# Kernel optimization log

Measured on AMD Instinct MI355X. Metric: run time of the kernel, lower is better.

The kernel has to match this reference:

```python
import jax, jax.numpy as jnp
import numpy as np

B, N, C = 8, 1024, 768
H = 12
HD = C // H
RANK = 8
SCALE = HD ** -0.5


def setup_inputs() -> dict:
    key = jax.random.key(0)
    ks = jax.random.split(key, 12)
    s = C ** -0.5
    inp = {
        'x': jax.random.normal(ks[0], (B, N, C), jnp.float32),
        'w_qkv': jax.random.normal(ks[1], (3 * C, C), jnp.float32) * s,
        'b_qkv': jax.random.normal(ks[2], (3 * C,), jnp.float32) * 0.02,
        'w_proj': jax.random.normal(ks[3], (C, C), jnp.float32) * s,
        'b_proj': jax.random.normal(ks[4], (C,), jnp.float32) * 0.02,
        # LoRA A matrices (kaiming-uniform-ish); B matrices are zero at init,
        # but use small nonzero values so the adapter path is exercised.
        'q_a': jax.random.normal(ks[5], (RANK, C), jnp.float32) * s,
        'q_b': jax.random.normal(ks[6], (C, RANK), jnp.float32) * 0.01,
        'k_a': jax.random.normal(ks[7], (RANK, C), jnp.float32) * s,
        'k_b': jax.random.normal(ks[8], (C, RANK), jnp.float32) * 0.01,
        'v_a': jax.random.normal(ks[9], (RANK, C), jnp.float32) * s,
        'v_b': jax.random.normal(ks[10], (C, RANK), jnp.float32) * 0.01,
        'o_a': jax.random.normal(ks[11], (RANK, C), jnp.float32) * s,
        'o_b': jax.random.normal(jax.random.fold_in(key, 99), (C, RANK), jnp.float32) * 0.01,
    }
    return inp


def _lora(x, wa, wb):
    # x:[B,N,C], wa:[r,C], wb:[C,r] -> [B,N,C]
    return jnp.einsum('bnr,cr->bnc', jnp.einsum('bnc,rc->bnr', x, wa), wb)


def reference(x, w_qkv, b_qkv, w_proj, b_proj, q_a, q_b, k_a, k_b, v_a, v_b, o_a, o_b):
    # QKV projection + fused LoRA slice-adds
    qkv = jnp.einsum('bnc,dc->bnd', x, w_qkv) + b_qkv  # [B,N,3C]
    q = qkv[:, :, :C] + _lora(x, q_a, q_b)
    k = qkv[:, :, C:2 * C] + _lora(x, k_a, k_b)
    v = qkv[:, :, 2 * C:] + _lora(x, v_a, v_b)
    # [B,H,N,HD]
    q = q.reshape(B, N, H, HD).transpose(0, 2, 1, 3)
    k = k.reshape(B, N, H, HD).transpose(0, 2, 1, 3)
    v = v.reshape(B, N, H, HD).transpose(0, 2, 1, 3)
    attn = jnp.einsum('bhqd,bhkd->bhqk', q, k) * SCALE
    attn = jax.nn.softmax(attn, axis=-1)  # dropout is identity in eval
    o = jnp.einsum('bhqk,bhkd->bhqd', attn, v)
    o = o.transpose(0, 2, 1, 3).reshape(B, N, C)
    out = jnp.einsum('bnc,dc->bnd', o, w_proj) + b_proj + _lora(o, o_a, o_b)
    return out
```

## Files before the change

### kernel.cpp

```cpp
#include <hip/hip_runtime.h>

typedef __attribute__((ext_vector_type(8))) short short8;
typedef __attribute__((ext_vector_type(4))) float f32x4;
typedef __attribute__((ext_vector_type(4))) unsigned short u16x4;
typedef __attribute__((ext_vector_type(2))) unsigned int u32x2;

#define MFMA16(a,b,c) __builtin_amdgcn_mfma_f32_16x16x32_bf16((a),(b),(c),0,0,0)

#define QSCALE 0.1803368801f

__device__ __forceinline__ unsigned short f2bf(float f) {
  unsigned int x = __float_as_uint(f);
  x += 0x7fffu + ((x >> 16) & 1u);
  return (unsigned short)(x >> 16);
}
__device__ __forceinline__ unsigned int pack2bf(float a, float b) {
  unsigned int ua = __float_as_uint(a) + 0x8000u;
  unsigned int ub = __float_as_uint(b) + 0x8000u;
  return __builtin_amdgcn_perm(ub, ua, 0x07060302);
}
__device__ __forceinline__ void gload16(const unsigned short* g, unsigned short* l) {
  __builtin_amdgcn_global_load_lds(
      (const __attribute__((address_space(1))) unsigned int*)g,
      (__attribute__((address_space(3))) unsigned int*)l, 16, 0, 0);
}

__global__ __launch_bounds__(256) void prep(
    const float* __restrict__ x,
    const float* __restrict__ w_qkv,
    const float* __restrict__ w_proj,
    const float* __restrict__ q_a, const float* __restrict__ q_b,
    const float* __restrict__ k_a, const float* __restrict__ k_b,
    const float* __restrict__ v_a, const float* __restrict__ v_b,
    const float* __restrict__ o_a, const float* __restrict__ o_b,
    unsigned short* __restrict__ xb,
    unsigned short* __restrict__ wqkv_eff,
    unsigned short* __restrict__ wproj_eff)
{
  int bid = blockIdx.x;
  if (bid < 6144) {
    int i4 = (bid * 256 + threadIdx.x) * 4;
    f32x4 v = *(const f32x4*)&x[i4];
    u16x4 o;
    o.x = f2bf(v.x); o.y = f2bf(v.y); o.z = f2bf(v.z); o.w = f2bf(v.w);
    *(u16x4*)&xb[i4] = o;
    return;
  }
  const int QKV = 2304 * 768;
  int idx = (bid - 6144) * 256 + threadIdx.x;
  if (idx < QKV) {
    int n = idx / 768, c = idx - n * 768;
    int sec = n / 768;
    int nr = n - sec * 768;
    const float* a; const float* b;
    if (sec == 0)      { a = q_a; b = q_b; }
    else if (sec == 1) { a = k_a; b = k_b; }
    else               { a = v_a; b = v_b; }
    float acc = w_qkv[idx];
    #pragma unroll
    for (int r = 0; r < 8; r++)
      acc += b[nr * 8 + r] * a[r * 768 + c];
    wqkv_eff[idx] = f2bf(acc);
  } else {
    int i2 = idx - QKV;
    int n = i2 / 768, c = i2 - n * 768;
    float acc = w_proj[i2];
    #pragma unroll
    for (int r = 0; r < 8; r++)
      acc += o_b[n * 8 + r] * o_a[r * 768 + c];
    wproj_eff[i2] = f2bf(acc);
  }
}

__global__ __launch_bounds__(256) void gemm_bt(
    const unsigned short* __restrict__ A,
    const unsigned short* __restrict__ W,
    const float* __restrict__ bias,
    unsigned short* __restrict__ out0,
    unsigned short* __restrict__ out1,
    unsigned short* __restrict__ out2,
    float* __restrict__ outf,
    int K, int Ncols, int mode)
{
  __shared__ alignas(16) unsigned short As[128][72];
  __shared__ alignas(16) unsigned short Ws[64][72];
  const int tid  = threadIdx.x;
  const int wave = tid >> 6;
  const int lane = tid & 63;
  const int quad = lane >> 4;
  const int l16  = lane & 15;
  const int m0 = blockIdx.x * 128;
  const int n0 = blockIdx.y * 64;

  int ar[4], ac[4], wr[2], wc[2];
  #pragma unroll
  for (int i = 0; i < 4; i++) { int f = tid + i * 256; ar[i] = f >> 3; ac[i] = (f & 7) << 3; }
  #pragma unroll
  for (int i = 0; i < 2; i++) { int f = tid + i * 256; wr[i] = f >> 3; wc[i] = (f & 7) << 3; }

  f32x4 areg[4], wreg[2];
  #pragma unroll
  for (int i = 0; i < 4; i++)
    areg[i] = *(const f32x4*)&A[(size_t)(m0 + ar[i]) * K + ac[i]];
  #pragma unroll
  for (int i = 0; i < 2; i++)
    wreg[i] = *(const f32x4*)&W[(size_t)(n0 + wr[i]) * K + wc[i]];

  f32x4 acc[2][4] = {};

  for (int k0 = 0; k0 < K; k0 += 64) {
    __syncthreads();
    #pragma unroll
    for (int i = 0; i < 4; i++) *(f32x4*)&As[ar[i]][ac[i]] = areg[i];
    #pragma unroll
    for (int i = 0; i < 2; i++) *(f32x4*)&Ws[wr[i]][wc[i]] = wreg[i];
    __syncthreads();
    if (k0 + 64 < K) {
      #pragma unroll
      for (int i = 0; i < 4; i++)
        areg[i] = *(const f32x4*)&A[(size_t)(m0 + ar[i]) * K + k0 + 64 + ac[i]];
      #pragma unroll
      for (int i = 0; i < 2; i++)
        wreg[i] = *(const f32x4*)&W[(size_t)(n0 + wr[i]) * K + k0 + 64 + wc[i]];
    }
    #pragma unroll
    for (int ks = 0; ks < 2; ks++) {
      const int kk = ks * 32 + quad * 8;
      short8 a0 = *(const short8*)&As[wave * 32 + l16][kk];
      short8 a1 = *(const short8*)&As[wave * 32 + 16 + l16][kk];
      short8 b0 = *(const short8*)&Ws[l16][kk];
      short8 b1 = *(const short8*)&Ws[16 + l16][kk];
      short8 b2 = *(const short8*)&Ws[32 + l16][kk];
      short8 b3 = *(const short8*)&Ws[48 + l16][kk];
      acc[0][0] = MFMA16(a0, b0, acc[0][0]);
      acc[0][1] = MFMA16(a0, b1, acc[0][1]);
      acc[0][2] = MFMA16(a0, b2, acc[0][2]);
      acc[0][3] = MFMA16(a0, b3, acc[0][3]);
      acc[1][0] = MFMA16(a1, b0, acc[1][0]);
      acc[1][1] = MFMA16(a1, b1, acc[1][1]);
      acc[1][2] = MFMA16(a1, b2, acc[1][2]);
      acc[1][3] = MFMA16(a1, b3, acc[1][3]);
    }
  }

  float bv[4];
  #pragma unroll
  for (int j = 0; j < 4; j++) bv[j] = bias[n0 + j * 16 + l16];

  if (mode == 0) {
    const int sec = n0 / 768;
    const int h   = (n0 % 768) >> 6;
    unsigned short* dst = (sec == 0) ? out0 : ((sec == 1) ? out1 : out2);
    const float scl = (sec == 0) ? QSCALE : 1.0f;
    #pragma unroll
    for (int rg = 0; rg < 2; rg++) {
      #pragma unroll
      for (int r = 0; r < 4; r++) {
        int m  = m0 + wave * 32 + rg * 16 + quad * 4 + r;
        int b  = m >> 10, np = m & 1023;
        int bh = b * 12 + h;
        int npp = (np & ~63) | ((np & 15) * 4 + ((np >> 4) & 3));
        #pragma unroll
        for (int j = 0; j < 4; j++) {
          int d = j * 16 + l16;
          float v = (acc[rg][j][r] + bv[j]) * scl;
          if (sec < 2) dst[((size_t)bh << 16) + ((size_t)np << 6) + d] = f2bf(v);
          else         dst[((size_t)bh << 16) + ((size_t)d << 10) + npp] = f2bf(v);
        }
      }
    }
  } else {
    #pragma unroll
    for (int rg = 0; rg < 2; rg++) {
      #pragma unroll
      for (int r = 0; r < 4; r++) {
        int m = m0 + wave * 32 + rg * 16 + quad * 4 + r;
        #pragma unroll
        for (int j = 0; j < 4; j++)
          outf[(size_t)m * Ncols + n0 + j * 16 + l16] = acc[rg][j][r] + bv[j];
      }
    }
  }
}

__global__ __launch_bounds__(256) void attn(
    const unsigned short* __restrict__ q,
    const unsigned short* __restrict__ k,
    const unsigned short* __restrict__ vt,
    unsigned short* __restrict__ o)
{
  __shared__ alignas(16) unsigned short Qs[128][72];
  __shared__ alignas(16) unsigned short Ks2[2][64 * 64];
  __shared__ alignas(16) unsigned short Vs2[2][64 * 64];
  const int tid  = threadIdx.x;
  const int wave = tid >> 6;
  const int lane = tid & 63;
  const int quad = lane >> 4;
  const int l16  = lane & 15;
  const int bh = blockIdx.x;
  const int q0 = blockIdx.y * 128;
  const unsigned short* qb = q  + ((size_t)bh << 16);
  const unsigned short* kb = k  + ((size_t)bh << 16);
  const unsigned short* vb = vt + ((size_t)bh << 16);

  const int lrow   = lane >> 3;
  const int lchunk = (lane & 7) ^ lrow;
  const unsigned short* gK[2];
  const unsigned short* gV[2];
  int lsKV[2];
  #pragma unroll
  for (int t = 0; t < 2; t++) {
    int rr = wave * 16 + t * 8 + lrow;
    gK[t]   = kb + (size_t)rr * 64 + lchunk * 8;
    gV[t]   = vb + (size_t)rr * 1024 + lchunk * 8;
    lsKV[t] = rr * 64 + (lane & 7) * 8;
  }
  const int swz = l16 & 7;

  #pragma unroll
  for (int t = 0; t < 2; t++) {
    gload16(gK[t], &Ks2[0][lsKV[t]]);
    gload16(gV[t], &Vs2[0][lsKV[t]]);
  }

  #pragma unroll
  for (int i = 0; i < 4; i++) {
    int flat = tid + i * 256;
    int r = flat >> 3, ck = (flat & 7) << 3;
    *(f32x4*)&Qs[r][ck] = *(const f32x4*)&qb[((size_t)(q0 + r) << 6) + ck];
  }
  __syncthreads();
  short8 aq[2][2];
  #pragma unroll
  for (int rg = 0; rg < 2; rg++)
    #pragma unroll
    for (int ks = 0; ks < 2; ks++)
      aq[rg][ks] = *(const short8*)&Qs[wave * 32 + rg * 16 + l16][ks * 32 + quad * 8];
  unsigned short (*Ps)[72] = (unsigned short (*)[72])(&Qs[wave * 32][0]);

  f32x4 Oacc[2][4] = {};
  float lsum[2][4] = {};

  for (int kt = 0; kt < 16; kt++) {
    const int p = kt & 1;
    __syncthreads();
    if (kt < 15) {
      #pragma unroll
      for (int t = 0; t < 2; t++) {
        gload16(gK[t] + (kt + 1) * 4096, &Ks2[1 - p][lsKV[t]]);
        gload16(gV[t] + (kt + 1) * 64,   &Vs2[1 - p][lsKV[t]]);
      }
    }

    f32x4 s[2][4] = {};
    #pragma unroll
    for (int ks = 0; ks < 2; ks++) {
      const int cs = ks * 4 + quad;
      short8 b0 = *(const short8*)&Ks2[p][(l16)      * 64 + ((cs ^ swz) << 3)];
      short8 b1 = *(const short8*)&Ks2[p][(16 + l16) * 64 + ((cs ^ swz) << 3)];
      short8 b2 = *(const short8*)&Ks2[p][(32 + l16) * 64 + ((cs ^ swz) << 3)];
      short8 b3 = *(const short8*)&Ks2[p][(48 + l16) * 64 + ((cs ^ swz) << 3)];
      s[0][0] = MFMA16(aq[0][ks], b0, s[0][0]);
      s[0][1] = MFMA16(aq[0][ks], b1, s[0][1]);
      s[0][2] = MFMA16(aq[0][ks], b2, s[0][2]);
      s[0][3] = MFMA16(aq[0][ks], b3, s[0][3]);
      s[1][0] = MFMA16(aq[1][ks], b0, s[1][0]);
      s[1][1] = MFMA16(aq[1][ks], b1, s[1][1]);
      s[1][2] = MFMA16(aq[1][ks], b2, s[1][2]);
      s[1][3] = MFMA16(aq[1][ks], b3, s[1][3]);
    }

    #pragma unroll
    for (int rg = 0; rg < 2; rg++) {
      #pragma unroll
      for (int r = 0; r < 4; r++) {
        float p0 = exp2f(s[rg][0][r]);
        float p1 = exp2f(s[rg][1][r]);
        float p2 = exp2f(s[rg][2][r]);
        float p3 = exp2f(s[rg][3][r]);
        lsum[rg][r] += (p0 + p1) + (p2 + p3);
        u32x2 pk;
        pk.x = pack2bf(p0, p1);
        pk.y = pack2bf(p2, p3);
        *(u32x2*)&Ps[rg * 16 + quad * 4 + r][4 * l16] = pk;
      }
    }

    #pragma unroll
    for (int ks = 0; ks < 2; ks++) {
      const int kk = ks * 32 + quad * 8;
      const int cs = ks * 4 + quad;
      short8 a0 = *(const short8*)&Ps[l16][kk];
      short8 a1 = *(const short8*)&Ps[16 + l16][kk];
      short8 v0 = *(const short8*)&Vs2[p][(l16)      * 64 + ((cs ^ swz) << 3)];
      short8 v1 = *(const short8*)&Vs2[p][(16 + l16) * 64 + ((cs ^ swz) << 3)];
      short8 v2 = *(const short8*)&Vs2[p][(32 + l16) * 64 + ((cs ^ swz) << 3)];
      short8 v3 = *(const short8*)&Vs2[p][(48 + l16) * 64 + ((cs ^ swz) << 3)];
      Oacc[0][0] = MFMA16(a0, v0, Oacc[0][0]);
      Oacc[0][1] = MFMA16(a0, v1, Oacc[0][1]);
      Oacc[0][2] = MFMA16(a0, v2, Oacc[0][2]);
      Oacc[0][3] = MFMA16(a0, v3, Oacc[0][3]);
      Oacc[1][0] = MFMA16(a1, v0, Oacc[1][0]);
      Oacc[1][1] = MFMA16(a1, v1, Oacc[1][1]);
      Oacc[1][2] = MFMA16(a1, v2, Oacc[1][2]);
      Oacc[1][3] = MFMA16(a1, v3, Oacc[1][3]);
    }
  }

  const int b = bh / 12, h = bh - (bh / 12) * 12;
  #pragma unroll
  for (int rg = 0; rg < 2; rg++) {
    #pragma unroll
    for (int r = 0; r < 4; r++) {
      float t = lsum[rg][r];
      t += __shfl_xor(t, 1, 64);
      t += __shfl_xor(t, 2, 64);
      t += __shfl_xor(t, 4, 64);
      t += __shfl_xor(t, 8, 64);
      float inv = 1.0f / t;
      int np = q0 + wave * 32 + rg * 16 + quad * 4 + r;
      size_t base = ((size_t)(b * 1024 + np)) * 768 + h * 64;
      #pragma unroll
      for (int j = 0; j < 4; j++)
        o[base + j * 16 + l16] = f2bf(Oacc[rg][j][r] * inv);
    }
  }
}

extern "C" void kernel_launch(void* const* d_in, const int* in_sizes, int n_in,
                              void* d_out, int out_size, void* d_ws, size_t ws_size,
                              hipStream_t stream) {
  const float* x      = (const float*)d_in[0];
  const float* w_qkv  = (const float*)d_in[1];
  const float* b_qkv  = (const float*)d_in[2];
  const float* w_proj = (const float*)d_in[3];
  const float* b_proj = (const float*)d_in[4];
  const float* q_a    = (const float*)d_in[5];
  const float* q_b    = (const float*)d_in[6];
  const float* k_a    = (const float*)d_in[7];
  const float* k_b    = (const float*)d_in[8];
  const float* v_a    = (const float*)d_in[9];
  const float* v_b    = (const float*)d_in[10];
  const float* o_a    = (const float*)d_in[11];
  const float* o_b    = (const float*)d_in[12];

  char* ws = (char*)d_ws;
  unsigned short* wqkv_eff  = (unsigned short*)(ws + 0);
  unsigned short* wproj_eff = (unsigned short*)(ws + 3538944);
  unsigned short* xb        = (unsigned short*)(ws + 4718592);
  unsigned short* qd        = (unsigned short*)(ws + 17301504);
  unsigned short* kd        = (unsigned short*)(ws + 29884416);
  unsigned short* vtd       = (unsigned short*)(ws + 42467328);
  unsigned short* od        = xb;

  prep<<<dim3(6144 + 9216), dim3(256), 0, stream>>>(
      x, w_qkv, w_proj, q_a, q_b, k_a, k_b, v_a, v_b, o_a, o_b,
      xb, wqkv_eff, wproj_eff);

  gemm_bt<<<dim3(64, 36), dim3(256), 0, stream>>>(
      xb, wqkv_eff, b_qkv, qd, kd, vtd, nullptr, 768, 2304, 0);

  attn<<<dim3(96, 8), dim3(256), 0, stream>>>(qd, kd, vtd, od);

  gemm_bt<<<dim3(64, 12), dim3(256), 0, stream>>>(
      od, wproj_eff, b_proj, nullptr, nullptr, nullptr, (float*)d_out, 768, 768, 1);
}
```

Baseline: 226.3 us.

## Store GEMM A operands in MFMA fragment layout and load directly to registers

Result: no change. 223.5 us (-1.2%).

```diff
diff --git a/kernel.cpp b/kernel.cpp
--- a/kernel.cpp
+++ b/kernel.cpp
@@ -24,6 +24,7 @@
       (const __attribute__((address_space(1))) unsigned int*)g,
       (__attribute__((address_space(3))) unsigned int*)l, 16, 0, 0);
 }
+
 
 __global__ __launch_bounds__(256) void prep(
     const float* __restrict__ x,
@@ -33,17 +34,22 @@
     const float* __restrict__ k_a, const float* __restrict__ k_b,
     const float* __restrict__ v_a, const float* __restrict__ v_b,
     const float* __restrict__ o_a, const float* __restrict__ o_b,
-    unsigned short* __restrict__ xb,
+    unsigned short* __restrict__ xf,
     unsigned short* __restrict__ wqkv_eff,
     unsigned short* __restrict__ wproj_eff)
 {
   int bid = blockIdx.x;
   if (bid < 6144) {
     int i4 = (bid * 256 + threadIdx.x) * 4;
+    int m  = i4 / 768;
+    int k4 = i4 - m * 768;
     f32x4 v = *(const f32x4*)&x[i4];
     u16x4 o;
     o.x = f2bf(v.x); o.y = f2bf(v.y); o.z = f2bf(v.z); o.w = f2bf(v.w);
-    *(u16x4*)&xb[i4] = o;
+    int kb = k4 >> 5, qd = (k4 >> 3) & 3, j0 = k4 & 7;
+    size_t idx = ((size_t)(kb * 512 + (m >> 4)) << 9) +
+                 (((qd << 4) + (m & 15)) << 3) + j0;
+    *(u16x4*)&xf[idx] = o;
     return;
   }
   const int QKV = 2304 * 768;
@@ -73,7 +79,7 @@
 }
 
 __global__ __launch_bounds__(256) void gemm_bt(
-    const unsigned short* __restrict__ A,
+    const unsigned short* __restrict__ Af,
     const unsigned short* __restrict__ W,
     const float* __restrict__ bias,
     unsigned short* __restrict__ out0,
@@ -82,7 +88,6 @@
     float* __restrict__ outf,
     int K, int Ncols, int mode)
 {
-  __shared__ alignas(16) unsigned short As[128][72];
   __shared__ alignas(16) unsigned short Ws[64][72];
   const int tid  = threadIdx.x;
   const int wave = tid >> 6;
@@ -91,56 +96,63 @@
   const int l16  = lane & 15;
   const int m0 = blockIdx.x * 128;
   const int n0 = blockIdx.y * 64;
-
-  int ar[4], ac[4], wr[2], wc[2];
-  #pragma unroll
-  for (int i = 0; i < 4; i++) { int f = tid + i * 256; ar[i] = f >> 3; ac[i] = (f & 7) << 3; }
+  const int M16b = (m0 >> 4) + wave * 2;
+
+  int wr[2], wc[2];
   #pragma unroll
   for (int i = 0; i < 2; i++) { int f = tid + i * 256; wr[i] = f >> 3; wc[i] = (f & 7) << 3; }
 
-  f32x4 areg[4], wreg[2];
-  #pragma unroll
-  for (int i = 0; i < 4; i++)
-    areg[i] = *(const f32x4*)&A[(size_t)(m0 + ar[i]) * K + ac[i]];
+  f32x4 wreg[2];
   #pragma unroll
   for (int i = 0; i < 2; i++)
     wreg[i] = *(const f32x4*)&W[(size_t)(n0 + wr[i]) * K + wc[i]];
 
+  short8 aCur[2][2], aNxt[2][2] = {};
+  #pragma unroll
+  for (int t = 0; t < 2; t++)
+    #pragma unroll
+    for (int ks = 0; ks < 2; ks++)
+      aCur[t][ks] = *(const short8*)&Af[((size_t)(ks * 512 + M16b + t) << 9) + (lane << 3)];
+
   f32x4 acc[2][4] = {};
 
   for (int k0 = 0; k0 < K; k0 += 64) {
     __syncthreads();
-    #pragma unroll
-    for (int i = 0; i < 4; i++) *(f32x4*)&As[ar[i]][ac[i]] = areg[i];
     #pragma unroll
     for (int i = 0; i < 2; i++) *(f32x4*)&Ws[wr[i]][wc[i]] = wreg[i];
     __syncthreads();
     if (k0 + 64 < K) {
       #pragma unroll
-      for (int i = 0; i < 4; i++)
-        areg[i] = *(const f32x4*)&A[(size_t)(m0 + ar[i]) * K + k0 + 64 + ac[i]];
-      #pragma unroll
       for (int i = 0; i < 2; i++)
         wreg[i] = *(const f32x4*)&W[(size_t)(n0 + wr[i]) * K + k0 + 64 + wc[i]];
+      const int kbn = (k0 + 64) >> 5;
+      #pragma unroll
+      for (int t = 0; t < 2; t++)
+        #pragma unroll
+        for (int ks = 0; ks < 2; ks++)
+          aNxt[t][ks] = *(const short8*)&Af[((size_t)((kbn + ks) * 512 + M16b + t) << 9) + (lane << 3)];
     }
     #pragma unroll
     for (int ks = 0; ks < 2; ks++) {
       const int kk = ks * 32 + quad * 8;
-      short8 a0 = *(const short8*)&As[wave * 32 + l16][kk];
-      short8 a1 = *(const short8*)&As[wave * 32 + 16 + l16][kk];
       short8 b0 = *(const short8*)&Ws[l16][kk];
       short8 b1 = *(const short8*)&Ws[16 + l16][kk];
       short8 b2 = *(const short8*)&Ws[32 + l16][kk];
       short8 b3 = *(const short8*)&Ws[48 + l16][kk];
-      acc[0][0] = MFMA16(a0, b0, acc[0][0]);
-      acc[0][1] = MFMA16(a0, b1, acc[0][1]);
-      acc[0][2] = MFMA16(a0, b2, acc[0][2]);
-      acc[0][3] = MFMA16(a0, b3, acc[0][3]);
-      acc[1][0] = MFMA16(a1, b0, acc[1][0]);
-      acc[1][1] = MFMA16(a1, b1, acc[1][1]);
-      acc[1][2] = MFMA16(a1, b2, acc[1][2]);
-      acc[1][3] = MFMA16(a1, b3, acc[1][3]);
-    }
+      acc[0][0] = MFMA16(aCur[0][ks], b0, acc[0][0]);
+      acc[0][1] = MFMA16(aCur[0][ks], b1, acc[0][1]);
+      acc[0][2] = MFMA16(aCur[0][ks], b2, acc[0][2]);
+      acc[0][3] = MFMA16(aCur[0][ks], b3, acc[0][3]);
+      acc[1][0] = MFMA16(aCur[1][ks], b0, acc[1][0]);
+      acc[1][1] = MFMA16(aCur[1][ks], b1, acc[1][1]);
+      acc[1][2] = MFMA16(aCur[1][ks], b2, acc[1][2]);
+      acc[1][3] = MFMA16(aCur[1][ks], b3, acc[1][3]);
+    }
+    #pragma unroll
+    for (int t = 0; t < 2; t++)
+      #pragma unroll
+      for (int ks = 0; ks < 2; ks++)
+        aCur[t][ks] = aNxt[t][ks];
   }
 
   float bv[4];
@@ -187,7 +199,7 @@
     const unsigned short* __restrict__ q,
     const unsigned short* __restrict__ k,
     const unsigned short* __restrict__ vt,
-    unsigned short* __restrict__ o)
+    unsigned short* __restrict__ of)
 {
   __shared__ alignas(16) unsigned short Qs[128][72];
   __shared__ alignas(16) unsigned short Ks2[2][64 * 64];
@@ -318,11 +330,18 @@
       t += __shfl_xor(t, 4, 64);
       t += __shfl_xor(t, 8, 64);
       float inv = 1.0f / t;
-      int np = q0 + wave * 32 + rg * 16 + quad * 4 + r;
-      size_t base = ((size_t)(b * 1024 + np)) * 768 + h * 64;
-      #pragma unroll
-      for (int j = 0; j < 4; j++)
-        o[base + j * 16 + l16] = f2bf(Oacc[rg][j][r] * inv);
+      int np  = q0 + wave * 32 + rg * 16 + quad * 4 + r;
+      int M16 = b * 64 + (np >> 4);
+      int l16m = np & 15;
+      #pragma unroll
+      for (int j = 0; j < 4; j++) {
+        int col = h * 64 + j * 16 + l16;
+        int kb2 = col >> 5;
+        int qc  = (col >> 3) & 3;
+        size_t idx = ((size_t)(kb2 * 512 + M16) << 9) +
+                     ((qc * 16 + l16m) << 3) + (l16 & 7);
+        of[idx] = f2bf(Oacc[rg][j][r] * inv);
+      }
     }
   }
 }
@@ -347,21 +366,21 @@
   char* ws = (char*)d_ws;
   unsigned short* wqkv_eff  = (unsigned short*)(ws + 0);
   unsigned short* wproj_eff = (unsigned short*)(ws + 3538944);
-  unsigned short* xb        = (unsigned short*)(ws + 4718592);
+  unsigned short* xf        = (unsigned short*)(ws + 4718592);
   unsigned short* qd        = (unsigned short*)(ws + 17301504);
   unsigned short* kd        = (unsigned short*)(ws + 29884416);
   unsigned short* vtd       = (unsigned short*)(ws + 42467328);
-  unsigned short* od        = xb;
+  unsigned short* of        = xf;
 
   prep<<<dim3(6144 + 9216), dim3(256), 0, stream>>>(
       x, w_qkv, w_proj, q_a, q_b, k_a, k_b, v_a, v_b, o_a, o_b,
-      xb, wqkv_eff, wproj_eff);
+      xf, wqkv_eff, wproj_eff);
 
   gemm_bt<<<dim3(64, 36), dim3(256), 0, stream>>>(
-      xb, wqkv_eff, b_qkv, qd, kd, vtd, nullptr, 768, 2304, 0);
-
-  attn<<<dim3(96, 8), dim3(256), 0, stream>>>(qd, kd, vtd, od);
+      xf, wqkv_eff, b_qkv, qd, kd, vtd, nullptr, 768, 2304, 0);
+
+  attn<<<dim3(96, 8), dim3(256), 0, stream>>>(qd, kd, vtd, of);
 
   gemm_bt<<<dim3(64, 12), dim3(256), 0, stream>>>(
-      od, wproj_eff, b_proj, nullptr, nullptr, nullptr, (float*)d_out, 768, 768, 1);
-}
+      of, wproj_eff, b_proj, nullptr, nullptr, nullptr, (float*)d_out, 768, 768, 1);
+}
```
